# Optimization experiments

Measured on AMD Instinct MI355X. Metric: run time of the kernel, lower is better.

The kernel has to match this reference:

```python
import jax, jax.numpy as jnp
import numpy as np

B, L, DIM, H, DQK, DV = 4, 512, 1024, 8, 64, 64
ANGLE_BASE = 1.0 / 1024.0
EPS = 1e-5


def _xavier(key, out_d, in_d, gain):
    bound = gain * np.sqrt(6.0 / (in_d + out_d))
    return jax.random.uniform(key, (out_d, in_d), jnp.float32, -bound, bound)


def setup_inputs():
    key = jax.random.key(0)
    ks = jax.random.split(key, 9)
    # p_angle buffer: angle_base ** linspace(0,1,H*DQK) reshaped to [H, DQK]
    p_angle = (ANGLE_BASE ** jnp.linspace(0.0, 1.0, H * DQK)).reshape(H, DQK)
    return {
        "x": jax.random.normal(ks[0], (B, L, DIM), jnp.float32),
        "hidden": 0.1 * jax.random.normal(ks[1], (B, H, DQK, DV, 2), jnp.float32),
        "w_qk": _xavier(ks[2], H * DQK * 4, DIM, 0.01), "b_qk": jnp.zeros((H * DQK * 4,), jnp.float32),
        "w_v": _xavier(ks[3], H * DV * 2, DIM, 0.01), "b_v": jnp.zeros((H * DV * 2,), jnp.float32),
        "w_g": _xavier(ks[4], H * DV * 2, DIM, 0.01), "b_g": jnp.zeros((H * DV * 2,), jnp.float32),
        "w_a": _xavier(ks[5], H, DIM, 1e-4), "b_a": jnp.zeros((H,), jnp.float32),
        "w_y": _xavier(ks[6], DIM, H * DV * 2, 0.01), "b_y": jnp.zeros((DIM,), jnp.float32),
        "gn_w": jnp.ones((H,), jnp.float32), "gn_b": jnp.zeros((H,), jnp.float32),
        "p_angle": p_angle,
    }


def _sioconv(x, hidden, w_qk, b_qk, w_v, b_v, w_g, b_g, w_a, b_a, w_y, b_y, gn_w, gn_b, p_angle):
    b, l = x.shape[0], x.shape[1]
    hid = hidden[..., 0] + 1j * hidden[..., 1]                       # [B,H,I,V] complex
    v_r = (x @ w_v.T + b_v).reshape(b, l, H, DV, 2)
    v = v_r[..., 0] + 1j * v_r[..., 1]                                # [B,L,H,V]
    qk_r = (x @ w_qk.T + b_qk).reshape(b, l, H, DQK, 2, 2)
    qk = qk_r[..., 0] + 1j * qk_r[..., 1]                             # [B,L,H,I,2]
    q, k = qk[..., 0], qk[..., 1]
    a_angle = x @ w_a.T + b_a                                         # [B,L,H]
    ln_a = (1j * a_angle - 1.0) * p_angle[:, 0]                       # [B,L,H] complex
    t = jnp.arange(l, dtype=jnp.float32)
    ppq = jnp.exp(1j * (t[:, None, None] * p_angle[None]))            # [L,H,I] = exp(+i*angle*l)
    qp = q * ppq[None]
    kp = k * jnp.conj(ppq)[None]                                      # exp(-i*angle*l)
    # Decay matrix. The FFT conv with ones computes a causal prefix sum, so
    # c[b,h,l,m] = exp(sum_{j=m+1..l} ln_a[b,j,h]) for m<=l, else 0.
    S = jnp.cumsum(ln_a, axis=1)                                      # [B,L,H]
    Sh = jnp.transpose(S, (0, 2, 1))                                  # [B,H,L]
    mask = jnp.tril(jnp.ones((l, l), bool))
    diff = jnp.where(mask, Sh[:, :, :, None] - Sh[:, :, None, :], 0.0)
    c = jnp.where(mask, jnp.exp(diff), 0.0)                           # [B,H,L,L]
    qck = jnp.einsum('blhi,bmhi->bhlm', qp, kp) * c
    h_inner = jnp.einsum('bhlm,bmhv->blhv', qck, v)
    d = jnp.exp(S)                                                    # [B,L,H] cumulative decay
    p1 = jnp.exp(1j * p_angle)                                        # [H,I]
    h_cross = jnp.einsum('blhi,bhiv->blhv', qp * d[..., None], hid * p1[None, :, :, None])
    h = h_inner + h_cross                                             # [B,L,H,V]
    pp_inv = jnp.exp(1j * ((l - 1.0 - t)[:, None, None] * p_angle[None]))  # [L,H,I]
    hid_next = jnp.einsum('blhi,bhl,lhi,blhv->bhiv', k, c[:, :, -1, :], pp_inv, v)
    hid_next = hid_next + jnp.exp(S[:, -1, :])[:, :, None, None] * hid * jnp.exp(1j * p_angle * l)[None, :, :, None]
    # GroupNorm(num_head, num_head) on real view [B*L, H, V, 2]: normalize over (V,2) per head.
    hr = jnp.stack([h.real, h.imag], axis=-1)                         # [B,L,H,V,2]
    mu = hr.mean(axis=(3, 4), keepdims=True)
    var = hr.var(axis=(3, 4), keepdims=True)
    hn = (hr - mu) / jnp.sqrt(var + EPS)
    hn = hn * gn_w[None, None, :, None, None] + gn_b[None, None, :, None, None]
    h_flat = hn.reshape(b, l, H * DV * 2)
    g = x @ w_g.T + b_g
    y = (h_flat * (g * jax.nn.sigmoid(g))) @ w_y.T + b_y
    return y, hid_next


def reference(x, hidden, w_qk, b_qk, w_v, b_v, w_g, b_g, w_a, b_a, w_y, b_y, gn_w, gn_b, p_angle):
    return _sioconv(x, hidden, w_qk, b_qk, w_v, b_v, w_g, b_g, w_a, b_a, w_y, b_y, gn_w, gn_b, p_angle)
```

## Files before the change

### kernel.cpp

```cpp
#include <hip/hip_runtime.h>
#include <cstdint>
#include <cstddef>

#define B_   4
#define L_   512
#define DIM_ 1024
#define H_   8
#define DQK_ 64
#define DV_  64
#define M_   (B_ * L_)
#define EPS_ 1e-5f

typedef __attribute__((ext_vector_type(8))) short short8;
typedef __attribute__((ext_vector_type(4))) float f32x4;

__device__ __forceinline__ unsigned short f2bf(float f) {
    uint32_t u = __float_as_uint(f);
    u += 0x7FFFu + ((u >> 16) & 1u);
    return (unsigned short)(u >> 16);
}
__device__ __forceinline__ float bf2f(unsigned short u) {
    return __uint_as_float((uint32_t)u << 16);
}

__device__ __forceinline__ f32x4 mm16(short8 a, short8 b, f32x4 c) {
    return __builtin_amdgcn_mfma_f32_16x16x32_bf16(a, b, c, 0, 0, 0);
}

__device__ __forceinline__ int swoff(int r, int kb) {
    return r * 128 + (kb ^ ((r & 7) << 4));
}
__device__ __forceinline__ short8 frag(const unsigned short* p, int strip, int ks, int lane) {
    const int fr = lane & 15, fq = lane >> 4;
    const int r = strip * 16 + fr;
    return *(const short8*)((const char*)p + swoff(r, ks * 64 + fq * 16));
}

__global__ __launch_bounds__(256) void cast_all(
    const float* __restrict__ x, const float* __restrict__ wqk,
    const float* __restrict__ wv, const float* __restrict__ wg,
    const float* __restrict__ wy, const float* __restrict__ wa,
    const float* __restrict__ ba,
    unsigned short* __restrict__ xb, unsigned short* __restrict__ wall,
    unsigned short* __restrict__ wyb, float* __restrict__ babias)
{
    const int blk = blockIdx.x;
    if (blk == 7176) {
        if (threadIdx.x < 128)
            babias[threadIdx.x] = (threadIdx.x < 8) ? ba[threadIdx.x] : 0.f;
        return;
    }
    const float* src; unsigned short* dst; int base;
    if      (blk < 2048) { src = x;   dst = xb;                  base = blk; }
    else if (blk < 4096) { src = wqk; dst = wall;                base = blk - 2048; }
    else if (blk < 5120) { src = wv;  dst = wall + 2048 * 1024;  base = blk - 4096; }
    else if (blk < 6144) { src = wg;  dst = wall + 3072 * 1024;  base = blk - 5120; }
    else if (blk < 7168) { src = wy;  dst = wyb;                 base = blk - 6144; }
    else                 { src = wa;  dst = wall + 4096 * 1024;  base = blk - 7168; }
    const int i = base * 256 + threadIdx.x;
    const float4 v = ((const float4*)src)[i];
    ushort4 o;
    o.x = f2bf(v.x); o.y = f2bf(v.y); o.z = f2bf(v.z); o.w = f2bf(v.w);
    ((ushort4*)dst)[i] = o;
}

__device__ __forceinline__ void gload16(const void* g, void* l) {
    __builtin_amdgcn_global_load_lds(
        (const __attribute__((address_space(1))) unsigned int*)g,
        (__attribute__((address_space(3))) unsigned int*)l, 16, 0, 0);
}

__global__ __launch_bounds__(256) void gemm_proj(
    const unsigned short* __restrict__ A, const unsigned short* __restrict__ W,
    const float* __restrict__ bias0, const float* __restrict__ bias1,
    const float* __restrict__ bias2, const float* __restrict__ bias3,
    void* __restrict__ C0, void* __restrict__ C1,
    void* __restrict__ C2, void* __restrict__ C3,
    int n1, int n2, int n3,
    int ld0, int ld1, int ld2, int ld3,
    int bf0, int bf1, int bf2, int bf3,
    int M, int N, int K)
{
    __shared__ unsigned short sA[128 * 32];
    __shared__ unsigned short sB[128 * 32];

    const int t    = threadIdx.x;
    const int lane = t & 63;
    const int wv   = t >> 6;
    const int bm   = blockIdx.y * 128;
    const int bn   = blockIdx.x * 128;
    const int wr   = wv >> 1, wc = wv & 1;
    const int fr   = lane & 15;
    const int fq   = lane >> 4;
    const int srow = lane >> 2;
    const int ske  = (lane & 3) * 8;

    f32x4 acc[4][4] = {};

    for (int k0 = 0; k0 < K; k0 += 32) {
#pragma unroll
        for (int q = 0; q < 2; ++q) {
            const int c2 = wv * 2 + q;
            gload16(A + (size_t)(bm + c2 * 16 + srow) * K + k0 + ske,
                    (char*)sA + c2 * 1024);
            gload16(W + (size_t)(bn + c2 * 16 + srow) * K + k0 + ske,
                    (char*)sB + c2 * 1024);
        }
        __syncthreads();

        short8 af[4], bf[4];
#pragma unroll
        for (int mi = 0; mi < 4; ++mi)
            af[mi] = *(const short8*)&sA[(wr * 64 + mi * 16 + fr) * 32 + fq * 8];
#pragma unroll
        for (int ni = 0; ni < 4; ++ni)
            bf[ni] = *(const short8*)&sB[(wc * 64 + ni * 16 + fr) * 32 + fq * 8];
#pragma unroll
        for (int mi = 0; mi < 4; ++mi)
#pragma unroll
            for (int ni = 0; ni < 4; ++ni)
                acc[mi][ni] = mm16(af[mi], bf[ni], acc[mi][ni]);
        __syncthreads();
    }

    void* Cb; const float* bb; int coff, ldc, isbf;
    if      (bn < n1) { Cb = C0; bb = bias0; coff = 0;  ldc = ld0; isbf = bf0; }
    else if (bn < n2) { Cb = C1; bb = bias1; coff = n1; ldc = ld1; isbf = bf1; }
    else if (bn < n3) { Cb = C2; bb = bias2; coff = n2; ldc = ld2; isbf = bf2; }
    else              { Cb = C3; bb = bias3; coff = n3; ldc = ld3; isbf = bf3; }

#pragma unroll
    for (int mi = 0; mi < 4; ++mi)
#pragma unroll
        for (int ni = 0; ni < 4; ++ni) {
            const int col = bn + wc * 64 + ni * 16 + fr - coff;
            const float bv = bb[col];
#pragma unroll
            for (int r = 0; r < 4; ++r) {
                const int row = bm + wr * 64 + mi * 16 + fq * 4 + r;
                const float val = acc[mi][ni][r] + bv;
                if (isbf)
                    ((unsigned short*)Cb)[(size_t)row * ldc + col] = f2bf(val);
                else
                    ((float*)Cb)[(size_t)row * ldc + col] = val;
            }
        }
}

__global__ __launch_bounds__(256) void gemm_y64(
    const unsigned short* __restrict__ A, const unsigned short* __restrict__ W,
    const float* __restrict__ bias, float* __restrict__ C,
    int M, int N, int K)
{
    __shared__ unsigned short sA[128 * 32];
    __shared__ unsigned short sB[64 * 32];

    const int t    = threadIdx.x;
    const int lane = t & 63;
    const int wv   = t >> 6;
    const int bm   = blockIdx.y * 128;
    const int bn   = blockIdx.x * 64;
    const int fr   = lane & 15;
    const int fq   = lane >> 4;
    const int srow = lane >> 2;
    const int ske  = (lane & 3) * 8;

    f32x4 acc[2][4] = {};

    for (int k0 = 0; k0 < K; k0 += 32) {
#pragma unroll
        for (int q = 0; q < 2; ++q) {
            const int c2 = wv * 2 + q;
            gload16(A + (size_t)(bm + c2 * 16 + srow) * K + k0 + ske,
                    (char*)sA + c2 * 1024);
        }
        gload16(W + (size_t)(bn + wv * 16 + srow) * K + k0 + ske,
                (char*)sB + wv * 1024);
        __syncthreads();

        short8 af[2], bf[4];
#pragma unroll
        for (int mi = 0; mi < 2; ++mi)
            af[mi] = *(const short8*)&sA[(wv * 32 + mi * 16 + fr) * 32 + fq * 8];
#pragma unroll
        for (int ni = 0; ni < 4; ++ni)
            bf[ni] = *(const short8*)&sB[(ni * 16 + fr) * 32 + fq * 8];
#pragma unroll
        for (int mi = 0; mi < 2; ++mi)
#pragma unroll
            for (int ni = 0; ni < 4; ++ni)
                acc[mi][ni] = mm16(af[mi], bf[ni], acc[mi][ni]);
        __syncthreads();
    }

#pragma unroll
    for (int mi = 0; mi < 2; ++mi)
#pragma unroll
        for (int ni = 0; ni < 4; ++ni) {
            const int col = bn + ni * 16 + fr;
            const float bv = bias[col];
#pragma unroll
            for (int r = 0; r < 4; ++r) {
                const int row = bm + wv * 32 + mi * 16 + fq * 4 + r;
                C[(size_t)row * N + col] = acc[mi][ni][r] + bv;
            }
        }
}

__global__ __launch_bounds__(256) void chunkA_mfma(
    const unsigned short* __restrict__ qk_bf, const unsigned short* __restrict__ v_bf,
    const float* __restrict__ a_pad, const float* __restrict__ p_angle,
    float* __restrict__ h_pre, float* __restrict__ Zloc,
    float* __restrict__ Gbuf, float* __restrict__ Wbuf)
{
    const int blk = blockIdx.x;
    const int c  = blk & 7;
    const int bh = blk >> 3;
    const int b = bh >> 3, h = bh & 7;
    const int t = threadIdx.x;
    const int l0 = c * 64;

    __shared__ unsigned short pQr[4096], pQi[4096];
    __shared__ unsigned short pKr[4096], pKi[4096];
    __shared__ unsigned short pKtr[4096], pKti[4096];
    __shared__ unsigned short pVtr[4096], pVti[4096];
    __shared__ float sW[64][4];
    __shared__ float sTh[64];

    if (t < 64) {
        sTh[t] = p_angle[h * DQK_ + t];
        const float th0 = p_angle[h * DQK_];
        const float a = a_pad[((size_t)(b * L_) + l0 + t) * 128 + h];
        float sa, ca; __sincosf(a * th0, &sa, &ca);
        const float em = expf(-th0), ep = expf(th0);
        float lr = em * ca, li = em * sa;
        float ir = ep * ca, ii = -ep * sa;
#pragma unroll
        for (int off = 1; off < 64; off <<= 1) {
            const float plr = __shfl_up(lr, off);
            const float pli = __shfl_up(li, off);
            const float pir = __shfl_up(ir, off);
            const float pii = __shfl_up(ii, off);
            if (t >= off) {
                float nr = lr * plr - li * pli;
                float ni = lr * pli + li * plr;
                lr = nr; li = ni;
                nr = ir * pir - ii * pii;
                ni = ir * pii + ii * pir;
                ir = nr; ii = ni;
            }
        }
        sW[t][0] = lr; sW[t][1] = li; sW[t][2] = ir; sW[t][3] = ii;
        Wbuf[((size_t)bh * L_ + l0 + t) * 2 + 0] = lr;
        Wbuf[((size_t)bh * L_ + l0 + t) * 2 + 1] = li;
        if (t == 63) {
            Gbuf[(bh * 8 + c) * 2 + 0] = lr;
            Gbuf[(bh * 8 + c) * 2 + 1] = li;
        }
    }
    __syncthreads();

    const int row = t >> 2, cs = t & 3;
    {
        const float wr = sW[row][0], wi = sW[row][1];
        const float xr = sW[row][2], xi = sW[row][3];
        const float lf = (float)(l0 + row);
        unsigned short qr16[16], qi16[16], kr16[16], ki16[16];
        const unsigned short* qg = qk_bf +
            (size_t)(b * L_ + l0 + row) * 2048 + h * 256 + cs * 64;
#pragma unroll
        for (int j = 0; j < 16; ++j) {
            const ushort4 qu = *(const ushort4*)(qg + j * 4);
            const float qre = bf2f(qu.x), qim = bf2f(qu.y);
            const float kre = bf2f(qu.z), kim = bf2f(qu.w);
            float sn, cn; __sincosf(sTh[cs * 16 + j] * lf, &sn, &cn);
            const float fqr = cn * wr - sn * wi, fqi = cn * wi + sn * wr;
            const float fkr = cn * xr + sn * xi, fki = cn * xi - sn * xr;
            qr16[j] = f2bf(qre * fqr - qim * fqi);
            qi16[j] = f2bf(qre * fqi + qim * fqr);
            const float kr = kre * fkr - kim * fki;
            const float ki = kre * fki + kim * fkr;
            kr16[j] = f2bf(kr); ki16[j] = f2bf(ki);
            const int i = cs * 16 + j;
            const int ob = swoff(i, 2 * row);
            *(unsigned short*)((char*)pKtr + ob) = kr16[j];
            *(unsigned short*)((char*)pKti + ob) = ki16[j];
        }
        const int kb0 = 32 * cs;
        short8 s0, s1;
#pragma unroll
        for (int j = 0; j < 8; ++j) { s0[j] = (short)qr16[j]; s1[j] = (short)qr16[8 + j]; }
        *(short8*)((char*)pQr + swoff(row, kb0))      = s0;
        *(short8*)((char*)pQr + swoff(row, kb0 + 16)) = s1;
#pragma unroll
        for (int j = 0; j < 8; ++j) { s0[j] = (short)qi16[j]; s1[j] = (short)qi16[8 + j]; }
        *(short8*)((char*)pQi + swoff(row, kb0))      = s0;
        *(short8*)((char*)pQi + swoff(row, kb0 + 16)) = s1;
#pragma unroll
        for (int j = 0; j < 8; ++j) { s0[j] = (short)kr16[j]; s1[j] = (short)kr16[8 + j]; }
        *(short8*)((char*)pKr + swoff(row, kb0))      = s0;
        *(short8*)((char*)pKr + swoff(row, kb0 + 16)) = s1;
#pragma unroll
        for (int j = 0; j < 8; ++j) { s0[j] = (short)ki16[j]; s1[j] = (short)ki16[8 + j]; }
        *(short8*)((char*)pKi + swoff(row, kb0))      = s0;
        *(short8*)((char*)pKi + swoff(row, kb0 + 16)) = s1;

        const unsigned short* vg = v_bf +
            (size_t)(b * L_ + l0 + row) * 1024 + h * 128 + cs * 32;
#pragma unroll
        for (int j = 0; j < 16; ++j) {
            const ushort2 vv = *(const ushort2*)(vg + j * 2);
            const int v = cs * 16 + j;
            const int ob = swoff(v, 2 * row);
            *(unsigned short*)((char*)pVtr + ob) = vv.x;
            *(unsigned short*)((char*)pVti + ob) = vv.y;
        }
    }
    __syncthreads();

    const int w = t >> 6, lane = t & 63;
    const int fr = lane & 15, fq = lane >> 4;
    short8 aQr0 = frag(pQr, w, 0, lane), aQr1 = frag(pQr, w, 1, lane);
    short8 aQi0 = frag(pQi, w, 0, lane), aQi1 = frag(pQi, w, 1, lane);
    f32x4 Pr[4], Pi[4];
#pragma unroll
    for (int tm = 0; tm < 4; ++tm) {
        short8 bKr0 = frag(pKr, tm, 0, lane), bKr1 = frag(pKr, tm, 1, lane);
        short8 bKi0 = frag(pKi, tm, 0, lane), bKi1 = frag(pKi, tm, 1, lane);
        f32x4 tmp = {};
        tmp = mm16(aQi0, bKi0, tmp); tmp = mm16(aQi1, bKi1, tmp);
        tmp = -tmp;
        tmp = mm16(aQr0, bKr0, tmp); tmp = mm16(aQr1, bKr1, tmp);
        Pr[tm] = tmp;
        f32x4 t2 = {};
        t2 = mm16(aQr0, bKi0, t2); t2 = mm16(aQr1, bKi1, t2);
        t2 = mm16(aQi0, bKr0, t2); t2 = mm16(aQi1, bKr1, t2);
        Pi[tm] = t2;
    }
#pragma unroll
    for (int tm = 0; tm < 4; ++tm) {
        const int m = tm * 16 + fr;
#pragma unroll
        for (int r = 0; r < 4; ++r) {
            const int l = w * 16 + fq * 4 + r;
            const int ob = swoff(l, 2 * m);
            const float prv = (m <= l) ? Pr[tm][r] : 0.f;
            const float piv = (m <= l) ? Pi[tm][r] : 0.f;
            *(unsigned short*)((char*)pQr + ob) = f2bf(prv);
            *(unsigned short*)((char*)pQi + ob) = f2bf(piv);
        }
    }

    short8 aPr0 = frag(pQr, w, 0, lane), aPr1 = frag(pQr, w, 1, lane);
    short8 aPi0 = frag(pQi, w, 0, lane), aPi1 = frag(pQi, w, 1, lane);
    short8 aKt_r0 = frag(pKtr, w, 0, lane), aKt_r1 = frag(pKtr, w, 1, lane);
    short8 aKt_i0 = frag(pKti, w, 0, lane), aKt_i1 = frag(pKti, w, 1, lane);
    const float Gr = sW[63][0], Gi = sW[63][1];
#pragma unroll
    for (int tv = 0; tv < 4; ++tv) {
        short8 bVr0 = frag(pVtr, tv, 0, lane), bVr1 = frag(pVtr, tv, 1, lane);
        short8 bVi0 = frag(pVti, tv, 0, lane), bVi1 = frag(pVti, tv, 1, lane);
        f32x4 hr = {};
        hr = mm16(aPi0, bVi0, hr); hr = mm16(aPi1, bVi1, hr);
        hr = -hr;
        hr = mm16(aPr0, bVr0, hr); hr = mm16(aPr1, bVr1, hr);
        f32x4 hi = {};
        hi = mm16(aPr0, bVi0, hi); hi = mm16(aPr1, bVi1, hi);
        hi = mm16(aPi0, bVr0, hi); hi = mm16(aPi1, bVr1, hi);
        f32x4 zr = {};
        zr = mm16(aKt_i0, bVi0, zr); zr = mm16(aKt_i1, bVi1, zr);
        zr = -zr;
        zr = mm16(aKt_r0, bVr0, zr); zr = mm16(aKt_r1, bVr1, zr);
        f32x4 zi = {};
        zi = mm16(aKt_r0, bVi0, zi); zi = mm16(aKt_r1, bVi1, zi);
        zi = mm16(aKt_i0, bVr0, zi); zi = mm16(aKt_i1, bVr1, zi);
#pragma unroll
        for (int r = 0; r < 4; ++r) {
            const int lrow = w * 16 + fq * 4 + r;
            const int v = tv * 16 + fr;
            *(float2*)(h_pre + (((size_t)(b * L_ + l0 + lrow) * H_ + h) * 64 + v) * 2)
                = make_float2(hr[r], hi[r]);
            float* zp = Zloc + (((size_t)(bh * 8 + c) * 4096) + lrow * 64 + v) * 2;
            zp[0] = Gr * zr[r] - Gi * zi[r];
            zp[1] = Gr * zi[r] + Gi * zr[r];
        }
    }
}

__global__ __launch_bounds__(512) void scanB(
    float* __restrict__ Zbuf, const float* __restrict__ Gbuf,
    const float* __restrict__ hidden, const float* __restrict__ p_angle,
    float* __restrict__ hid_out, int real_only)
{
    const int bid = blockIdx.x;
    const int bh = bid >> 3, part = bid & 7;
    const int h = bh & 7;
    const int e = part * 512 + threadIdx.x;
    const int i = e >> 6;
    const float th = p_angle[h * 64 + i];
    float s, c; __sincosf(th, &s, &c);
    const float2 h0 = *(const float2*)(hidden + ((size_t)bh * 4096 + e) * 2);
    float zr = h0.x * c - h0.y * s;
    float zi = h0.x * s + h0.y * c;
#pragma unroll
    for (int ch = 0; ch < 8; ++ch) {
        float* zp = Zbuf + ((size_t)(bh * 8 + ch) * 4096 + e) * 2;
        const float zlr = zp[0], zli = zp[1];
        zp[0] = zr; zp[1] = zi;
        const float gr = Gbuf[(bh * 8 + ch) * 2], gi = Gbuf[(bh * 8 + ch) * 2 + 1];
        const float nr = gr * zr - gi * zi + zlr;
        const float ni = gr * zi + gi * zr + zli;
        zr = nr; zi = ni;
    }
    float s2, c2; __sincosf(th * (float)(L_ - 1), &s2, &c2);
    const float outr = zr * c2 - zi * s2;
    const float outi = zr * s2 + zi * c2;
    if (real_only) {
        hid_out[(size_t)bh * 4096 + e] = outr;
    } else {
        hid_out[((size_t)bh * 4096 + e) * 2 + 0] = outr;
        hid_out[((size_t)bh * 4096 + e) * 2 + 1] = outi;
    }
}

__global__ __launch_bounds__(256) void chunkC_gn(
    const unsigned short* __restrict__ qk_bf, const float* __restrict__ Wbuf,
    const float* __restrict__ Zin, const float* __restrict__ p_angle,
    const float* __restrict__ h_intra, const float* __restrict__ gbuf,
    const float* __restrict__ gn_w, const float* __restrict__ gn_b,
    unsigned short* __restrict__ act)
{
    const int blk = blockIdx.x;
    const int c = blk & 7, bh = blk >> 3;
    const int b = bh >> 3, h = bh & 7;
    const int t = threadIdx.x;
    const int l0 = c * 64;

    __shared__ unsigned short pQr[4096], pQi[4096];
    __shared__ unsigned short pZtr[4096], pZti[4096];
    __shared__ float sTh[64];

    if (t < 64) sTh[t] = p_angle[h * 64 + t];
    __syncthreads();

    const int row = t >> 2, cs = t & 3;
    {
        const float wr = Wbuf[((size_t)bh * L_ + l0 + row) * 2];
        const float wi = Wbuf[((size_t)bh * L_ + l0 + row) * 2 + 1];
        const float lf = (float)(l0 + row);
        unsigned short qr16[16], qi16[16];
        const unsigned short* qg = qk_bf +
            (size_t)(b * L_ + l0 + row) * 2048 + h * 256 + cs * 64;
#pragma unroll
        for (int j = 0; j < 16; ++j) {
            const ushort4 qu = *(const ushort4*)(qg + j * 4);
            const float qre = bf2f(qu.x), qim = bf2f(qu.y);
            float sn, cn; __sincosf(sTh[cs * 16 + j] * lf, &sn, &cn);
            const float fqr = cn * wr - sn * wi, fqi = cn * wi + sn * wr;
            qr16[j] = f2bf(qre * fqr - qim * fqi);
            qi16[j] = f2bf(qre * fqi + qim * fqr);
        }
        const int kb0 = 32 * cs;
        short8 s0, s1;
#pragma unroll
        for (int j = 0; j < 8; ++j) { s0[j] = (short)qr16[j]; s1[j] = (short)qr16[8 + j]; }
        *(short8*)((char*)pQr + swoff(row, kb0))      = s0;
        *(short8*)((char*)pQr + swoff(row, kb0 + 16)) = s1;
#pragma unroll
        for (int j = 0; j < 8; ++j) { s0[j] = (short)qi16[j]; s1[j] = (short)qi16[8 + j]; }
        *(short8*)((char*)pQi + swoff(row, kb0))      = s0;
        *(short8*)((char*)pQi + swoff(row, kb0 + 16)) = s1;

        const float2* zg = (const float2*)(Zin +
            ((size_t)(bh * 8 + c) * 4096 + row * 64 + cs * 16) * 2);
#pragma unroll
        for (int j = 0; j < 16; ++j) {
            const float2 z = zg[j];
            const int v = cs * 16 + j;
            const int ob = swoff(v, 2 * row);
            *(unsigned short*)((char*)pZtr + ob) = f2bf(z.x);
            *(unsigned short*)((char*)pZti + ob) = f2bf(z.y);
        }
    }
    __syncthreads();

    const int w = t >> 6, lane = t & 63;
    const int fr = lane & 15, fq = lane >> 4;
    short8 aQr0 = frag(pQr, w, 0, lane), aQr1 = frag(pQr, w, 1, lane);
    short8 aQi0 = frag(pQi, w, 0, lane), aQi1 = frag(pQi, w, 1, lane);

    float hreg[4][4][2];
#pragma unroll
    for (int tv = 0; tv < 4; ++tv) {
        short8 bZr0 = frag(pZtr, tv, 0, lane), bZr1 = frag(pZtr, tv, 1, lane);
        short8 bZi0 = frag(pZti, tv, 0, lane), bZi1 = frag(pZti, tv, 1, lane);
        f32x4 hr = {};
        hr = mm16(aQi0, bZi0, hr); hr = mm16(aQi1, bZi1, hr);
        hr = -hr;
        hr = mm16(aQr0, bZr0, hr); hr = mm16(aQr1, bZr1, hr);
        f32x4 hi = {};
        hi = mm16(aQr0, bZi0, hi); hi = mm16(aQr1, bZi1, hi);
        hi = mm16(aQi0, bZr0, hi); hi = mm16(aQi1, bZr1, hi);
#pragma unroll
        for (int r = 0; r < 4; ++r) {
            const int l = w * 16 + fq * 4 + r;
            const int v = tv * 16 + fr;
            const float2 hin = *(const float2*)(h_intra +
                (((size_t)(b * L_ + l0 + l) * H_ + h) * 64 + v) * 2);
            hreg[tv][r][0] = hin.x + hr[r];
            hreg[tv][r][1] = hin.y + hi[r];
        }
    }

    const float gw = gn_w[h], gbn = gn_b[h];
    float mean4[4], scl4[4];
#pragma unroll
    for (int r = 0; r < 4; ++r) {
        float s = 0.f, q = 0.f;
#pragma unroll
        for (int tv = 0; tv < 4; ++tv) {
            s += hreg[tv][r][0] + hreg[tv][r][1];
            q += hreg[tv][r][0] * hreg[tv][r][0] + hreg[tv][r][1] * hreg[tv][r][1];
        }
#pragma unroll
        for (int off = 1; off < 16; off <<= 1) {
            s += __shfl_xor(s, off);
            q += __shfl_xor(q, off);
        }
        const float m = s * (1.f / 128.f);
        const float var = q * (1.f / 128.f) - m * m;
        mean4[r] = m;
        scl4[r] = rsqrtf(var + EPS_) * gw;
    }

#pragma unroll
    for (int tv = 0; tv < 4; ++tv) {
#pragma unroll
        for (int r = 0; r < 4; ++r) {
            const int l = w * 16 + fq * 4 + r;
            const int v = tv * 16 + fr;
            const size_t base = (size_t)(b * L_ + l0 + l) * 1024 + h * 128 + v * 2;
            const float2 gv = *(const float2*)(gbuf + base);
            const float hn0 = (hreg[tv][r][0] - mean4[r]) * scl4[r] + gbn;
            const float hn1 = (hreg[tv][r][1] - mean4[r]) * scl4[r] + gbn;
            const float a0 = hn0 * gv.x / (1.f + expf(-gv.x));
            const float a1 = hn1 * gv.y / (1.f + expf(-gv.y));
            ushort2 o; o.x = f2bf(a0); o.y = f2bf(a1);
            *(ushort2*)(act + base) = o;
        }
    }
}

extern "C" void kernel_launch(void* const* d_in, const int* in_sizes, int n_in,
                              void* d_out, int out_size, void* d_ws, size_t ws_size,
                              hipStream_t stream)
{
    (void)in_sizes; (void)n_in; (void)ws_size;
    const float* x       = (const float*)d_in[0];
    const float* hidden  = (const float*)d_in[1];
    const float* w_qk    = (const float*)d_in[2];
    const float* b_qk    = (const float*)d_in[3];
    const float* w_v     = (const float*)d_in[4];
    const float* b_v     = (const float*)d_in[5];
    const float* w_g     = (const float*)d_in[6];
    const float* b_g     = (const float*)d_in[7];
    const float* w_a     = (const float*)d_in[8];
    const float* b_a     = (const float*)d_in[9];
    const float* w_y     = (const float*)d_in[10];
    const float* b_y     = (const float*)d_in[11];
    const float* gn_w    = (const float*)d_in[12];
    const float* gn_b    = (const float*)d_in[13];
    const float* p_angle = (const float*)d_in[14];

    float* y_out   = (float*)d_out;
    float* hid_out = (float*)d_out + (size_t)M_ * DIM_;
    const int hid_elems = out_size - M_ * DIM_;
    const int real_only = (hid_elems == B_ * H_ * DQK_ * DV_) ? 1 : 0;

    unsigned short* xb     = (unsigned short*)d_ws;
    unsigned short* wall   = xb   + (size_t)2048 * 1024;
    unsigned short* wyb    = wall + (size_t)4224 * 1024;
    unsigned short* bqk    = wyb  + (size_t)1024 * 1024;
    unsigned short* bv     = bqk  + (size_t)2048 * 2048;
    unsigned short* actb   = bv   + (size_t)2048 * 1024;
    float* bg     = (float*)(actb + (size_t)2048 * 1024);
    float* ba_pad = bg     + (size_t)2048 * 1024;
    float* babias = ba_pad + (size_t)2048 * 128;
    float* bufW   = babias + 128;
    float* bufG   = bufW   + 32 * 512 * 2;
    float* bufZ   = bufG   + 512;
    float* bufh   = bufZ   + (size_t)32 * 8 * 4096 * 2;

    cast_all<<<7177, 256, 0, stream>>>(x, w_qk, w_v, w_g, w_y, w_a, b_a,
                                       xb, wall, wyb, babias);

    gemm_proj<<<dim3(33, 16), 256, 0, stream>>>(
        xb, wall, b_qk, b_v, b_g, babias,
        bqk, bv, bg, ba_pad,
        2048, 3072, 4096,
        2048, 1024, 1024, 128,
        1, 1, 0, 0,
        M_, 4224, DIM_);

    chunkA_mfma<<<B_*H_*8, 256, 0, stream>>>(
        bqk, bv, ba_pad, p_angle, bufh, bufZ, bufG, bufW);
    scanB<<<B_*H_*8, 512, 0, stream>>>(
        bufZ, bufG, hidden, p_angle, hid_out, real_only);
    chunkC_gn<<<B_*H_*8, 256, 0, stream>>>(
        bqk, bufW, bufZ, p_angle, bufh, bg, gn_w, gn_b, actb);

    gemm_y64<<<dim3(16, 16), 256, 0, stream>>>(
        actb, wyb, b_y, y_out, M_, DIM_, DIM_);
}
```

Baseline: 95.62 us.

## Spread GEMM tiles across more waves and blocks for higher occupancy

The projection GEMM now runs 8 waves per 128x128 tile instead of 4, so each wave computes a 64x32 sub-tile and issues one LDS-load per operand. The output GEMM drops to 64x64 tiles with 4 waves in a 2x2 layout, which doubles the grid to 512 blocks. Both changes aim to put more waves on each CU to hide latency and fill the 256 CUs. In exchange, each wave reuses less data from its fragments and the same data is loaded from global memory more often.

```diff
diff --git a/kernel.cpp b/kernel.cpp
--- a/kernel.cpp
+++ b/kernel.cpp
@@ -70,7 +70,7 @@
         (__attribute__((address_space(3))) unsigned int*)l, 16, 0, 0);
 }
 
-__global__ __launch_bounds__(256) void gemm_proj(
+__global__ __launch_bounds__(512) void gemm_proj(
     const unsigned short* __restrict__ A, const unsigned short* __restrict__ W,
     const float* __restrict__ bias0, const float* __restrict__ bias1,
     const float* __restrict__ bias2, const float* __restrict__ bias3,
@@ -89,36 +89,33 @@
     const int wv   = t >> 6;
     const int bm   = blockIdx.y * 128;
     const int bn   = blockIdx.x * 128;
-    const int wr   = wv >> 1, wc = wv & 1;
+    const int wr   = wv >> 2;
+    const int wc   = wv & 3;
     const int fr   = lane & 15;
     const int fq   = lane >> 4;
     const int srow = lane >> 2;
     const int ske  = (lane & 3) * 8;
 
-    f32x4 acc[4][4] = {};
+    f32x4 acc[4][2] = {};
 
     for (int k0 = 0; k0 < K; k0 += 32) {
-#pragma unroll
-        for (int q = 0; q < 2; ++q) {
-            const int c2 = wv * 2 + q;
-            gload16(A + (size_t)(bm + c2 * 16 + srow) * K + k0 + ske,
-                    (char*)sA + c2 * 1024);
-            gload16(W + (size_t)(bn + c2 * 16 + srow) * K + k0 + ske,
-                    (char*)sB + c2 * 1024);
-        }
+        gload16(A + (size_t)(bm + wv * 16 + srow) * K + k0 + ske,
+                (char*)sA + wv * 1024);
+        gload16(W + (size_t)(bn + wv * 16 + srow) * K + k0 + ske,
+                (char*)sB + wv * 1024);
         __syncthreads();
 
-        short8 af[4], bf[4];
+        short8 af[4], bf[2];
 #pragma unroll
         for (int mi = 0; mi < 4; ++mi)
             af[mi] = *(const short8*)&sA[(wr * 64 + mi * 16 + fr) * 32 + fq * 8];
 #pragma unroll
-        for (int ni = 0; ni < 4; ++ni)
-            bf[ni] = *(const short8*)&sB[(wc * 64 + ni * 16 + fr) * 32 + fq * 8];
+        for (int ni = 0; ni < 2; ++ni)
+            bf[ni] = *(const short8*)&sB[(wc * 32 + ni * 16 + fr) * 32 + fq * 8];
 #pragma unroll
         for (int mi = 0; mi < 4; ++mi)
 #pragma unroll
-            for (int ni = 0; ni < 4; ++ni)
+            for (int ni = 0; ni < 2; ++ni)
                 acc[mi][ni] = mm16(af[mi], bf[ni], acc[mi][ni]);
         __syncthreads();
     }
@@ -132,8 +129,8 @@
 #pragma unroll
     for (int mi = 0; mi < 4; ++mi)
 #pragma unroll
-        for (int ni = 0; ni < 4; ++ni) {
-            const int col = bn + wc * 64 + ni * 16 + fr - coff;
+        for (int ni = 0; ni < 2; ++ni) {
+            const int col = bn + wc * 32 + ni * 16 + fr - coff;
             const float bv = bb[col];
 #pragma unroll
             for (int r = 0; r < 4; ++r) {
@@ -147,48 +144,46 @@
         }
 }
 
-__global__ __launch_bounds__(256) void gemm_y64(
+__global__ __launch_bounds__(256) void gemm_y(
     const unsigned short* __restrict__ A, const unsigned short* __restrict__ W,
     const float* __restrict__ bias, float* __restrict__ C,
     int M, int N, int K)
 {
-    __shared__ unsigned short sA[128 * 32];
+    __shared__ unsigned short sA[64 * 32];
     __shared__ unsigned short sB[64 * 32];
 
     const int t    = threadIdx.x;
     const int lane = t & 63;
     const int wv   = t >> 6;
-    const int bm   = blockIdx.y * 128;
+    const int bm   = blockIdx.y * 64;
     const int bn   = blockIdx.x * 64;
+    const int wr   = wv >> 1;
+    const int wc   = wv & 1;
     const int fr   = lane & 15;
     const int fq   = lane >> 4;
     const int srow = lane >> 2;
     const int ske  = (lane & 3) * 8;
 
-    f32x4 acc[2][4] = {};
+    f32x4 acc[2][2] = {};
 
     for (int k0 = 0; k0 < K; k0 += 32) {
-#pragma unroll
-        for (int q = 0; q < 2; ++q) {
-            const int c2 = wv * 2 + q;
-            gload16(A + (size_t)(bm + c2 * 16 + srow) * K + k0 + ske,
-                    (char*)sA + c2 * 1024);
-        }
+        gload16(A + (size_t)(bm + wv * 16 + srow) * K + k0 + ske,
+                (char*)sA + wv * 1024);
         gload16(W + (size_t)(bn + wv * 16 + srow) * K + k0 + ske,
                 (char*)sB + wv * 1024);
         __syncthreads();
 
-        short8 af[2], bf[4];
+        short8 af[2], bf[2];
 #pragma unroll
         for (int mi = 0; mi < 2; ++mi)
-            af[mi] = *(const short8*)&sA[(wv * 32 + mi * 16 + fr) * 32 + fq * 8];
-#pragma unroll
-        for (int ni = 0; ni < 4; ++ni)
-            bf[ni] = *(const short8*)&sB[(ni * 16 + fr) * 32 + fq * 8];
+            af[mi] = *(const short8*)&sA[(wr * 32 + mi * 16 + fr) * 32 + fq * 8];
+#pragma unroll
+        for (int ni = 0; ni < 2; ++ni)
+            bf[ni] = *(const short8*)&sB[(wc * 32 + ni * 16 + fr) * 32 + fq * 8];
 #pragma unroll
         for (int mi = 0; mi < 2; ++mi)
 #pragma unroll
-            for (int ni = 0; ni < 4; ++ni)
+            for (int ni = 0; ni < 2; ++ni)
                 acc[mi][ni] = mm16(af[mi], bf[ni], acc[mi][ni]);
         __syncthreads();
     }
@@ -196,12 +191,12 @@
 #pragma unroll
     for (int mi = 0; mi < 2; ++mi)
 #pragma unroll
-        for (int ni = 0; ni < 4; ++ni) {
-            const int col = bn + ni * 16 + fr;
+        for (int ni = 0; ni < 2; ++ni) {
+            const int col = bn + wc * 32 + ni * 16 + fr;
             const float bv = bias[col];
 #pragma unroll
             for (int r = 0; r < 4; ++r) {
-                const int row = bm + wv * 32 + mi * 16 + fq * 4 + r;
+                const int row = bm + wr * 32 + mi * 16 + fq * 4 + r;
                 C[(size_t)row * N + col] = acc[mi][ni][r] + bv;
             }
         }
@@ -594,7 +589,7 @@
     cast_all<<<7177, 256, 0, stream>>>(x, w_qk, w_v, w_g, w_y, w_a, b_a,
                                        xb, wall, wyb, babias);
 
-    gemm_proj<<<dim3(33, 16), 256, 0, stream>>>(
+    gemm_proj<<<dim3(33, 16), 512, 0, stream>>>(
         xb, wall, b_qk, b_v, b_g, babias,
         bqk, bv, bg, ba_pad,
         2048, 3072, 4096,
@@ -609,6 +604,6 @@
     chunkC_gn<<<B_*H_*8, 256, 0, stream>>>(
         bqk, bufW, bufZ, p_angle, bufh, bg, gn_w, gn_b, actb);
 
-    gemm_y64<<<dim3(16, 16), 256, 0, stream>>>(
+    gemm_y<<<dim3(16, 32), 256, 0, stream>>>(
         actb, wyb, b_y, y_out, M_, DIM_, DIM_);
 }
```

Measured after the change: 89.79 us, median of 2. 6.1% less time.
